# Kernel optimization log

Measured on AMD Instinct MI355X. Metric: run time of the kernel, lower is better.

## Reference

```python
import jax, jax.numpy as jnp
import numpy as np

NUM_HEADS = 16
SLICE_SIZE = 1024
SCALING = SLICE_SIZE ** 0.5  # module divides by sqrt(slice_size), as written


def setup_inputs() -> dict:
    key = jax.random.key(0)
    ks = jax.random.split(key, 9)
    B, S, D = 4, 2048, SLICE_SIZE
    sc = 0.02
    return {
        "x": jax.random.normal(ks[0], (B, S, D), dtype=jnp.float32),
        "Wq": jax.random.normal(ks[1], (D, D), dtype=jnp.float32) * sc,
        "bq": jax.random.normal(ks[2], (D,), dtype=jnp.float32) * sc,
        "Wk": jax.random.normal(ks[3], (D, D), dtype=jnp.float32) * sc,
        "bk": jax.random.normal(ks[4], (D,), dtype=jnp.float32) * sc,
        "Wv": jax.random.normal(ks[5], (D, D), dtype=jnp.float32) * sc,
        "bv": jax.random.normal(ks[6], (D,), dtype=jnp.float32) * sc,
        "Wp": jax.random.normal(ks[7], (D, D), dtype=jnp.float32) * sc,
        "bp": jax.random.normal(ks[8], (D,), dtype=jnp.float32) * sc,
    }


def _split_heads(t):
    # 'b s (h o) -> b h s o'
    b, s, d = t.shape
    return t.reshape(b, s, NUM_HEADS, d // NUM_HEADS).transpose(0, 2, 1, 3)


def reference(x, Wq, bq, Wk, bk, Wv, bv, Wp, bp):
    q = _split_heads(x @ Wq.T + bq)  # [B,H,S,O]
    k = _split_heads(x @ Wk.T + bk)
    v = _split_heads(x @ Wv.T + bv)
    energy = jnp.einsum('bhqo,bhko->bhqk', q, k)  # full score matrix
    attn = jax.nn.softmax(energy / SCALING, axis=-1)
    # Faithful to source: 'b h q k, b h v o -> b h v o' sums attn over (q,k)
    out = jnp.einsum('bhqk,bhvo->bhvo', attn, v)
    b, h, s, o = out.shape
    out = out.transpose(0, 2, 1, 3).reshape(b, s, h * o)  # 'b h v o -> b v (h o)'
    return out @ Wp.T + bp
```

## Files before the change

### kernel.cpp

```cpp
#include <hip/hip_runtime.h>
#include <cstdint>


typedef unsigned short u16;
typedef __bf16 bf16x8 __attribute__((ext_vector_type(8)));
typedef float f32x4 __attribute__((ext_vector_type(4)));

__device__ __forceinline__ u16 f2bf(float f) {
  unsigned int u = __float_as_uint(f);
  u += 0x7fffu + ((u >> 16) & 1u);
  return (u16)(u >> 16);
}

__device__ __forceinline__ void load16(const void* g, void* l) {
  auto gp = (const __attribute__((address_space(1))) unsigned int*)(uintptr_t)g;
  auto lp = (__attribute__((address_space(3))) unsigned int*)(unsigned int)(uintptr_t)l;
  __builtin_amdgcn_global_load_lds(gp, lp, 16, 0, 0);
}

__global__ void k_prep(const float* __restrict__ x, const float* __restrict__ Wv,
                       const float* __restrict__ bv, const float* __restrict__ Wp,
                       const float* __restrict__ bp, u16* __restrict__ xb,
                       u16* __restrict__ wpb, u16* __restrict__ wvtb,
                       float* __restrict__ cv) {
  __shared__ float tile[32][33];
  const int b = blockIdx.x;
  const int tid = threadIdx.x;
  if (b < 9216) {
    const float* src = (b < 8192) ? x : Wp;
    u16* dst = (b < 8192) ? xb : wpb;
    const long base = (long)((b < 8192) ? b : (b - 8192)) * 1024 + tid * 4;
    const float4 v = *(const float4*)(src + base);
    ushort4 o;
    o.x = f2bf(v.x); o.y = f2bf(v.y); o.z = f2bf(v.z); o.w = f2bf(v.w);
    *(ushort4*)(dst + base) = o;
  } else if (b < 10240) {
    const int tb = b - 9216;
    const int bi = (tb & 31) * 32;
    const int bj = (tb >> 5) * 32;
    const int tx = tid & 31;
    const int ty = tid >> 5;
    for (int r = ty; r < 32; r += 8)
      tile[r][tx] = Wv[(long)(bj + r) * 1024 + bi + tx];
    __syncthreads();
    for (int r = ty; r < 32; r += 8)
      wvtb[(long)(bi + r) * 1024 + bj + tx] = f2bf(tile[tx][r]);
  } else {
    const int row = (b - 10240) * 4 + (tid >> 6);
    const int lane = tid & 63;
    const float* w = Wp + (long)row * 1024;
    float s = 0.f;
    for (int j = lane; j < 1024; j += 64) s += w[j] * bv[j];
    for (int off = 32; off; off >>= 1) s += __shfl_down(s, off, 64);
    if (lane == 0) cv[row] = 2048.f * s + bp[row];
  }
}

__global__ void k_reduce(const float* __restrict__ p, u16* __restrict__ dst) {
  const long i = (long)(blockIdx.x * 256 + threadIdx.x) * 4;
  const float4 a = *(const float4*)(p + i);
  const float4 b = *(const float4*)(p + 1048576 + i);
  const float4 c = *(const float4*)(p + 2097152 + i);
  const float4 d = *(const float4*)(p + 3145728 + i);
  ushort4 o;
  o.x = f2bf((a.x + b.x + c.x + d.x) * 2048.f);
  o.y = f2bf((a.y + b.y + c.y + d.y) * 2048.f);
  o.z = f2bf((a.z + b.z + c.z + d.z) * 2048.f);
  o.w = f2bf((a.w + b.w + c.w + d.w) * 2048.f);
  *(ushort4*)(dst + i) = o;
}

template <int BN, int MODE>
__global__ __launch_bounds__(256, BN == 64 ? 4 : 3) void k_gemm(
    const u16* __restrict__ A, const u16* __restrict__ B, float* __restrict__ Out,
    const float* __restrict__ bias, int M, int N, int K) {
  constexpr int NT = BN / 32;
  __shared__ u16 As[128 * 32];
  __shared__ u16 Bs[BN * 32];

  const int tid = threadIdx.x;
  const int lane = tid & 63;
  const int wv = tid >> 6;
  const int waveM = (wv & 1) << 6;
  const int waveN = (wv >> 1) * (BN / 2);
  const int l15 = lane & 15;
  const int quad = lane >> 4;

  const long bm = (long)blockIdx.x * 128;
  const long bn = (long)blockIdx.y * BN;
  const int kChunk = K / gridDim.z;
  const int kBeg = blockIdx.z * kChunk;
  const int kEnd = kBeg + kChunk;

  const int srow = tid >> 2;
  const int scol = (tid & 3) << 3;
  const u16* Ag = A + (bm + srow) * K + scol;
  const u16* Bg = B + (bn + srow) * K + scol;
  u16* As0 = As + wv * 512;
  u16* As1 = As + 2048 + wv * 512;
  u16* Bs0 = Bs + wv * 512;

  const f32x4 zero = {0.f, 0.f, 0.f, 0.f};
  f32x4 acc[4][NT];
#pragma unroll
  for (int i = 0; i < 4; ++i)
#pragma unroll
    for (int j = 0; j < NT; ++j) acc[i][j] = zero;

  for (int k0 = kBeg; k0 < kEnd; k0 += 32) {
    __syncthreads();
    load16(Ag + k0, As0);
    load16(Ag + (long)64 * K + k0, As1);
    load16(Bg + k0, Bs0);
    if constexpr (BN == 128) load16(Bg + (long)64 * K + k0, Bs + 2048 + wv * 512);
    __syncthreads();

    bf16x8 af[4], bg[NT];
#pragma unroll
    for (int t = 0; t < 4; ++t)
      af[t] = *(const bf16x8*)(As + (waveM + t * 16 + l15) * 32 + quad * 8);
#pragma unroll
    for (int t = 0; t < NT; ++t)
      bg[t] = *(const bf16x8*)(Bs + (waveN + t * 16 + l15) * 32 + quad * 8);
#pragma unroll
    for (int i = 0; i < 4; ++i)
#pragma unroll
      for (int j = 0; j < NT; ++j)
        acc[i][j] = __builtin_amdgcn_mfma_f32_16x16x32_bf16(af[i], bg[j], acc[i][j], 0, 0, 0);
  }

  float* outp = (MODE == 1) ? Out + (long)blockIdx.z * M * N : Out;
#pragma unroll
  for (int i = 0; i < 4; ++i) {
    const long gm = bm + waveM + i * 16 + quad * 4;
#pragma unroll
    for (int j = 0; j < NT; ++j) {
      const long gn = bn + waveN + j * 16 + l15;
      const float bb = (MODE == 0) ? bias[gn] : 0.f;
#pragma unroll
      for (int r = 0; r < 4; ++r)
        outp[(gm + r) * N + gn] = acc[i][j][r] + bb;
    }
  }
}

extern "C" void kernel_launch(void* const* d_in, const int* in_sizes, int n_in,
                              void* d_out, int out_size, void* d_ws, size_t ws_size,
                              hipStream_t stream) {
  const float* x  = (const float*)d_in[0];
  const float* Wv = (const float*)d_in[5];
  const float* bv = (const float*)d_in[6];
  const float* Wp = (const float*)d_in[7];
  const float* bp = (const float*)d_in[8];

  char* ws = (char*)d_ws;
  u16* xb    = (u16*)(ws);
  u16* wpb   = (u16*)(ws + (16u << 20));
  u16* wvtb  = (u16*)(ws + (18u << 20));
  u16* m2b   = (u16*)(ws + (20u << 20));
  float* cv  = (float*)(ws + (22u << 20));
  float* m2f = (float*)(ws + (22u << 20) + 4096);

  k_prep<<<10496, 256, 0, stream>>>(x, Wv, bv, Wp, bp, xb, wpb, wvtb, cv);

  k_gemm<128, 1><<<dim3(8, 8, 4), 256, 0, stream>>>(wpb, wvtb, m2f, nullptr,
                                                    1024, 1024, 1024);
  k_reduce<<<1024, 256, 0, stream>>>(m2f, m2b);

  k_gemm<64, 0><<<dim3(64, 16, 1), 256, 0, stream>>>(xb, m2b, (float*)d_out, cv,
                                                     8192, 1024, 1024);
}
```

Measured before the change: 149.0 us.

## Switch GEMM to 64x256 tiles with XCD-aware block swizzle

Replaces the 128xBN GEMM tile with a 64x256 tile in which each wave owns a 64x64 output block. For the main GEMM it also remaps the 1D block index so that consecutive blocks on the same XCD share A rows across the N tiles, aiming for better L2 reuse. The larger N tile raises B traffic per block and uses more LDS, and launch bounds drop to 3 blocks per CU for the main GEMM.

```diff
diff --git a/kernel.cpp b/kernel.cpp
--- a/kernel.cpp
+++ b/kernel.cpp
@@ -70,71 +70,79 @@
   *(ushort4*)(dst + i) = o;
 }
 
-template <int BN, int MODE>
-__global__ __launch_bounds__(256, BN == 64 ? 4 : 3) void k_gemm(
+template <int MODE, int NB>
+__global__ __launch_bounds__(256, 3) void k_gemm(
     const u16* __restrict__ A, const u16* __restrict__ B, float* __restrict__ Out,
     const float* __restrict__ bias, int M, int N, int K) {
-  constexpr int NT = BN / 32;
-  __shared__ u16 As[128 * 32];
-  __shared__ u16 Bs[BN * 32];
+  __shared__ u16 As[64 * 32];
+  __shared__ u16 Bs[256 * 32];
 
   const int tid = threadIdx.x;
   const int lane = tid & 63;
   const int wv = tid >> 6;
-  const int waveM = (wv & 1) << 6;
-  const int waveN = (wv >> 1) * (BN / 2);
+  const int waveN = wv << 6;
   const int l15 = lane & 15;
   const int quad = lane >> 4;
 
-  const long bm = (long)blockIdx.x * 128;
-  const long bn = (long)blockIdx.y * BN;
-  const int kChunk = K / gridDim.z;
-  const int kBeg = blockIdx.z * kChunk;
-  const int kEnd = kBeg + kChunk;
+  long bm, bn;
+  int kBeg, kEnd;
+  if constexpr (MODE == 0) {
+    const int id = blockIdx.x;
+    const int xcd = id & 7;
+    const int j = id >> 3;
+    const int mPerXcd = M / 64 / 8;
+    bm = (long)(xcd * mPerXcd + j / NB) * 64;
+    bn = (long)(j % NB) * 256;
+    kBeg = 0; kEnd = K;
+  } else {
+    bm = (long)blockIdx.x * 64;
+    bn = (long)blockIdx.y * 256;
+    const int kChunk = K / gridDim.z;
+    kBeg = blockIdx.z * kChunk;
+    kEnd = kBeg + kChunk;
+  }
 
   const int srow = tid >> 2;
   const int scol = (tid & 3) << 3;
   const u16* Ag = A + (bm + srow) * K + scol;
   const u16* Bg = B + (bn + srow) * K + scol;
   u16* As0 = As + wv * 512;
-  u16* As1 = As + 2048 + wv * 512;
   u16* Bs0 = Bs + wv * 512;
 
   const f32x4 zero = {0.f, 0.f, 0.f, 0.f};
-  f32x4 acc[4][NT];
+  f32x4 acc[4][4];
 #pragma unroll
   for (int i = 0; i < 4; ++i)
 #pragma unroll
-    for (int j = 0; j < NT; ++j) acc[i][j] = zero;
+    for (int j = 0; j < 4; ++j) acc[i][j] = zero;
 
   for (int k0 = kBeg; k0 < kEnd; k0 += 32) {
     __syncthreads();
     load16(Ag + k0, As0);
-    load16(Ag + (long)64 * K + k0, As1);
-    load16(Bg + k0, Bs0);
-    if constexpr (BN == 128) load16(Bg + (long)64 * K + k0, Bs + 2048 + wv * 512);
+#pragma unroll
+    for (int r = 0; r < 4; ++r)
+      load16(Bg + (long)r * 64 * K + k0, Bs0 + r * 2048);
     __syncthreads();
 
-    bf16x8 af[4], bg[NT];
+    bf16x8 af[4], bg[4];
 #pragma unroll
-    for (int t = 0; t < 4; ++t)
-      af[t] = *(const bf16x8*)(As + (waveM + t * 16 + l15) * 32 + quad * 8);
-#pragma unroll
-    for (int t = 0; t < NT; ++t)
+    for (int t = 0; t < 4; ++t) {
+      af[t] = *(const bf16x8*)(As + (t * 16 + l15) * 32 + quad * 8);
       bg[t] = *(const bf16x8*)(Bs + (waveN + t * 16 + l15) * 32 + quad * 8);
+    }
 #pragma unroll
     for (int i = 0; i < 4; ++i)
 #pragma unroll
-      for (int j = 0; j < NT; ++j)
+      for (int j = 0; j < 4; ++j)
         acc[i][j] = __builtin_amdgcn_mfma_f32_16x16x32_bf16(af[i], bg[j], acc[i][j], 0, 0, 0);
   }
 
   float* outp = (MODE == 1) ? Out + (long)blockIdx.z * M * N : Out;
 #pragma unroll
   for (int i = 0; i < 4; ++i) {
-    const long gm = bm + waveM + i * 16 + quad * 4;
+    const long gm = bm + i * 16 + quad * 4;
 #pragma unroll
-    for (int j = 0; j < NT; ++j) {
+    for (int j = 0; j < 4; ++j) {
       const long gn = bn + waveN + j * 16 + l15;
       const float bb = (MODE == 0) ? bias[gn] : 0.f;
 #pragma unroll
@@ -163,10 +171,10 @@
 
   k_prep<<<10496, 256, 0, stream>>>(x, Wv, bv, Wp, bp, xb, wpb, wvtb, cv);
 
-  k_gemm<128, 1><<<dim3(8, 8, 4), 256, 0, stream>>>(wpb, wvtb, m2f, nullptr,
-                                                    1024, 1024, 1024);
+  k_gemm<1, 4><<<dim3(16, 4, 4), 256, 0, stream>>>(wpb, wvtb, m2f, nullptr,
+                                                   1024, 1024, 1024);
   k_reduce<<<1024, 256, 0, stream>>>(m2f, m2b);
 
-  k_gemm<64, 0><<<dim3(64, 16, 1), 256, 0, stream>>>(xb, m2b, (float*)d_out, cv,
-                                                     8192, 1024, 1024);
+  k_gemm<0, 4><<<512, 256, 0, stream>>>(xb, m2b, (float*)d_out, cv,
+                                        8192, 1024, 1024);
 }
```

Result: slower. 153.5 us (+3.0%).
